# Kernel tuning notes

Measured on AMD Instinct MI355X. Metric: run time of the kernel, lower is better.

## Reference

```python
import jax, jax.numpy as jnp
import numpy as np

N = 50000      # nodes
E = 800000     # edges (avg degree 16)
F_IN = 64      # node_feature_space
H = 64         # hidden_dim
G = 16         # graphs in batch
BN_EPS = 1e-5


def setup_inputs() -> dict:
    key = jax.random.key(0)
    ks = jax.random.split(key, 8)
    x = jax.random.normal(ks[0], (N, F_IN), jnp.float32)
    edge_index = jax.random.randint(ks[1], (2, E), 0, N, dtype=jnp.int64)
    batch = jnp.sort(jax.random.randint(ks[2], (N,), 0, G, dtype=jnp.int64))
    init = lambda k, shp, fan: jax.random.normal(k, shp, jnp.float32) / np.float32(np.sqrt(fan))
    params = dict(
        W1_0=init(ks[3], (F_IN, H), F_IN), b1_0=jnp.zeros((H,), jnp.float32),
        W2_0=init(ks[4], (H, H), H),       b2_0=jnp.zeros((H,), jnp.float32),
        g_0=jnp.ones((H,), jnp.float32),   be_0=jnp.zeros((H,), jnp.float32),
        W1_1=init(ks[5], (H, H), H),       b1_1=jnp.zeros((H,), jnp.float32),
        W2_1=init(ks[6], (H, H), H),       b2_1=jnp.zeros((H,), jnp.float32),
        g_1=jnp.ones((H,), jnp.float32),   be_1=jnp.zeros((H,), jnp.float32),
    )
    return dict(x=x, edge_index=edge_index, batch=batch, **params)


def _gin_layer(x, src, dst, W1, b1, W2, b2, g, be):
    # GINConv (eps=0): h_i = MLP(x_i + sum_{j->i} x_j)
    agg = jax.ops.segment_sum(x[src], dst, num_segments=N)   # [N, d]
    h = x + agg
    h = jnp.maximum(h @ W1 + b1, 0.0) @ W2 + b2              # Linear-ReLU-Linear
    # BatchNorm1d (training-mode batch stats, biased variance as in torch)
    mu = h.mean(axis=0)
    var = h.var(axis=0)
    h = (h - mu) * jax.lax.rsqrt(var + BN_EPS) * g + be
    return jnp.maximum(h, 0.0)                               # ReLU


def reference(x, edge_index, batch,
              W1_0, b1_0, W2_0, b2_0, g_0, be_0,
              W1_1, b1_1, W2_1, b2_1, g_1, be_1):
    src, dst = edge_index[0], edge_index[1]
    x = _gin_layer(x, src, dst, W1_0, b1_0, W2_0, b2_0, g_0, be_0)
    x = _gin_layer(x, src, dst, W1_1, b1_1, W2_1, b2_1, g_1, be_1)
    # global_mean_pool over graph ids
    cnt = jax.ops.segment_sum(jnp.ones((N,), x.dtype), batch, num_segments=G)
    sums = jax.ops.segment_sum(x, batch, num_segments=G)
    h_graph = sums / jnp.maximum(cnt, 1.0)[:, None]
    return (x, h_graph)
```

## Files before the change

### kernel.cpp

```cpp
#include <hip/hip_runtime.h>
#include <hip/hip_bf16.h>


constexpr int NN = 50000;
constexpr int NE = 800000;
constexpr int HD = 64;
constexpr int NG = 16;
constexpr float BN_EPS = 1e-5f;
constexpr int ROWCAP = 64;
constexpr int NPART = 8;
constexpr int PSZ = 6250;

__device__ __forceinline__ int rdl(int v, int l) {
    return __builtin_amdgcn_readlane(v, l);
}

__global__ __launch_bounds__(256)
void prep_kernel(const float* __restrict__ x, __hip_bfloat16* __restrict__ xb,
                 int* __restrict__ cnt, float* __restrict__ stats0,
                 float* __restrict__ stats1, float* __restrict__ psums) {
    int i4 = blockIdx.x * 256 + threadIdx.x;
    if (i4 < NN) cnt[i4] = 0;
    if (blockIdx.x == 0) {
        if (threadIdx.x < 128) stats0[threadIdx.x] = 0.f;
        else stats1[threadIdx.x - 128] = 0.f;
    } else if (blockIdx.x == 1) {
        *(float4*)(psums + threadIdx.x * 4) = make_float4(0.f, 0.f, 0.f, 0.f);
    }
    if (i4 >= NN * HD / 4) return;
    float4 v = *(const float4*)(x + (size_t)i4 * 4);
    union { ushort4 u; __hip_bfloat16 b[4]; } p;
    p.b[0] = __float2bfloat16(v.x);
    p.b[1] = __float2bfloat16(v.y);
    p.b[2] = __float2bfloat16(v.z);
    p.b[3] = __float2bfloat16(v.w);
    *(ushort4*)((unsigned short*)xb + (size_t)i4 * 4) = p.u;
}

__global__ __launch_bounds__(256)
void scatter_kernel(const int* __restrict__ ei, int* __restrict__ cnt,
                    unsigned short* __restrict__ csr) {
    int p = blockIdx.x & 7;
    int chunk = blockIdx.x >> 3;
    int e4 = (chunk * 256 + threadIdx.x) * 4;
    if (e4 >= NE) return;
    int4 s = *(const int4*)(ei + e4);
    int4 d = *(const int4*)(ei + NE + e4);
    int lo = p * PSZ, hi = lo + PSZ;
    int slot;
    if (d.x >= lo && d.x < hi) {
        slot = atomicAdd(&cnt[d.x], 1);
        if (slot < ROWCAP) csr[(d.x << 6) + slot] = (unsigned short)s.x;
    }
    if (d.y >= lo && d.y < hi) {
        slot = atomicAdd(&cnt[d.y], 1);
        if (slot < ROWCAP) csr[(d.y << 6) + slot] = (unsigned short)s.y;
    }
    if (d.z >= lo && d.z < hi) {
        slot = atomicAdd(&cnt[d.z], 1);
        if (slot < ROWCAP) csr[(d.z << 6) + slot] = (unsigned short)s.z;
    }
    if (d.w >= lo && d.w < hi) {
        slot = atomicAdd(&cnt[d.w], 1);
        if (slot < ROWCAP) csr[(d.w << 6) + slot] = (unsigned short)s.w;
    }
}

template <int MODE>
__global__ __launch_bounds__(512)
void layer_kernel(const float* __restrict__ xin, const __hip_bfloat16* __restrict__ xg,
                  const int* __restrict__ cnt, const unsigned short* __restrict__ csr,
                  const float* __restrict__ stats_prev, const float* __restrict__ gp,
                  const float* __restrict__ bep,
                  const float* __restrict__ W1, const float* __restrict__ b1,
                  const float* __restrict__ W2, const float* __restrict__ b2,
                  float* __restrict__ hout, float* __restrict__ stats,
                  __hip_bfloat16* __restrict__ xbr) {
    __shared__ float sh[128 * 65];
    __shared__ float red[2][8][64];
    int tid = threadIdx.x;
    int base = blockIdx.x * 128;
    int w = tid >> 6, lane = tid & 63;
    int wu = __builtin_amdgcn_readfirstlane(w);

    float sc = 1.f, off = 0.f;
    if (MODE == 1) {
        const float inv = 1.f / (float)NN;
        float mu = stats_prev[lane] * inv;
        float var = stats_prev[64 + lane] * inv - mu * mu;
        sc = gp[lane] * rsqrtf(var + BN_EPS);
        off = bep[lane] - mu * sc;
    }

    for (int rl = wu * 16; rl < wu * 16 + 16; rl++) {
        int grow = base + rl;
        float acc = 0.f;
        if (grow < NN) {
            int m = min(cnt[grow], ROWCAP);
            int ids = (int)csr[((size_t)grow << 6) + lane];
            float sv = xin[(size_t)grow * HD + lane];
            acc = (MODE == 1) ? fmaxf(fmaf(sv, sc, off), 0.f) : sv;
            int j = 0;
            float a0 = 0.f, a1 = 0.f, a2 = 0.f, a3 = 0.f;
            float a4 = 0.f, a5 = 0.f, a6 = 0.f, a7 = 0.f;
            for (; j + 8 <= m; j += 8) {
                int n0 = rdl(ids, j);
                int n1 = rdl(ids, j + 1);
                int n2 = rdl(ids, j + 2);
                int n3 = rdl(ids, j + 3);
                int n4 = rdl(ids, j + 4);
                int n5 = rdl(ids, j + 5);
                int n6 = rdl(ids, j + 6);
                int n7 = rdl(ids, j + 7);
                float v0 = __bfloat162float(xg[((size_t)n0 << 6) + lane]);
                float v1 = __bfloat162float(xg[((size_t)n1 << 6) + lane]);
                float v2 = __bfloat162float(xg[((size_t)n2 << 6) + lane]);
                float v3 = __bfloat162float(xg[((size_t)n3 << 6) + lane]);
                float v4 = __bfloat162float(xg[((size_t)n4 << 6) + lane]);
                float v5 = __bfloat162float(xg[((size_t)n5 << 6) + lane]);
                float v6 = __bfloat162float(xg[((size_t)n6 << 6) + lane]);
                float v7 = __bfloat162float(xg[((size_t)n7 << 6) + lane]);
                if (MODE == 1) {
                    a0 += fmaxf(fmaf(v0, sc, off), 0.f);
                    a1 += fmaxf(fmaf(v1, sc, off), 0.f);
                    a2 += fmaxf(fmaf(v2, sc, off), 0.f);
                    a3 += fmaxf(fmaf(v3, sc, off), 0.f);
                    a4 += fmaxf(fmaf(v4, sc, off), 0.f);
                    a5 += fmaxf(fmaf(v5, sc, off), 0.f);
                    a6 += fmaxf(fmaf(v6, sc, off), 0.f);
                    a7 += fmaxf(fmaf(v7, sc, off), 0.f);
                } else {
                    a0 += v0; a1 += v1; a2 += v2; a3 += v3;
                    a4 += v4; a5 += v5; a6 += v6; a7 += v7;
                }
            }
            acc += ((a0 + a1) + (a2 + a3)) + ((a4 + a5) + (a6 + a7));
            for (; j < m; j++) {
                int nb = rdl(ids, j);
                float v = __bfloat162float(xg[((size_t)nb << 6) + lane]);
                acc += (MODE == 1) ? fmaxf(fmaf(v, sc, off), 0.f) : v;
            }
        }
        sh[rl * 65 + lane] = acc;
    }
    __syncthreads();

    float acc0[8], acc1[8];
#pragma unroll
    for (int j = 0; j < 8; j++) { acc0[j] = b1[wu * 8 + j]; acc1[j] = acc0[j]; }
    for (int k = 0; k < 64; k++) {
        float a0 = sh[lane * 65 + k];
        float a1 = sh[(64 + lane) * 65 + k];
        const float4* wr = (const float4*)(W1 + k * 64 + wu * 8);
#pragma unroll
        for (int q = 0; q < 2; q++) {
            float4 wv = wr[q];
            acc0[4 * q + 0] = fmaf(a0, wv.x, acc0[4 * q + 0]);
            acc0[4 * q + 1] = fmaf(a0, wv.y, acc0[4 * q + 1]);
            acc0[4 * q + 2] = fmaf(a0, wv.z, acc0[4 * q + 2]);
            acc0[4 * q + 3] = fmaf(a0, wv.w, acc0[4 * q + 3]);
            acc1[4 * q + 0] = fmaf(a1, wv.x, acc1[4 * q + 0]);
            acc1[4 * q + 1] = fmaf(a1, wv.y, acc1[4 * q + 1]);
            acc1[4 * q + 2] = fmaf(a1, wv.z, acc1[4 * q + 2]);
            acc1[4 * q + 3] = fmaf(a1, wv.w, acc1[4 * q + 3]);
        }
    }
    __syncthreads();

#pragma unroll
    for (int j = 0; j < 8; j++) {
        sh[lane * 65 + wu * 8 + j] = fmaxf(acc0[j], 0.f);
        sh[(64 + lane) * 65 + wu * 8 + j] = fmaxf(acc1[j], 0.f);
    }
    __syncthreads();

#pragma unroll
    for (int j = 0; j < 8; j++) { acc0[j] = b2[wu * 8 + j]; acc1[j] = acc0[j]; }
    for (int k = 0; k < 64; k++) {
        float a0 = sh[lane * 65 + k];
        float a1 = sh[(64 + lane) * 65 + k];
        const float4* wr = (const float4*)(W2 + k * 64 + wu * 8);
#pragma unroll
        for (int q = 0; q < 2; q++) {
            float4 wv = wr[q];
            acc0[4 * q + 0] = fmaf(a0, wv.x, acc0[4 * q + 0]);
            acc0[4 * q + 1] = fmaf(a0, wv.y, acc0[4 * q + 1]);
            acc0[4 * q + 2] = fmaf(a0, wv.z, acc0[4 * q + 2]);
            acc0[4 * q + 3] = fmaf(a0, wv.w, acc0[4 * q + 3]);
            acc1[4 * q + 0] = fmaf(a1, wv.x, acc1[4 * q + 0]);
            acc1[4 * q + 1] = fmaf(a1, wv.y, acc1[4 * q + 1]);
            acc1[4 * q + 2] = fmaf(a1, wv.z, acc1[4 * q + 2]);
            acc1[4 * q + 3] = fmaf(a1, wv.w, acc1[4 * q + 3]);
        }
    }
    __syncthreads();
#pragma unroll
    for (int j = 0; j < 8; j++) {
        sh[lane * 65 + wu * 8 + j] = acc0[j];
        sh[(64 + lane) * 65 + wu * 8 + j] = acc1[j];
    }
    __syncthreads();

#pragma unroll
    for (int i = 0; i < 4; i++) {
        int i4 = tid + 512 * i;
        int row = i4 >> 4, col = (i4 & 15) * 4;
        int grow = base + row;
        if (grow < NN) {
            const float* s = sh + row * 65 + col;
            float4 v = make_float4(s[0], s[1], s[2], s[3]);
            *(float4*)(hout + (size_t)grow * HD + col) = v;
            if (xbr) {
                union { ushort4 u; __hip_bfloat16 b[4]; } p;
                p.b[0] = __float2bfloat16(v.x);
                p.b[1] = __float2bfloat16(v.y);
                p.b[2] = __float2bfloat16(v.z);
                p.b[3] = __float2bfloat16(v.w);
                *(ushort4*)((unsigned short*)xbr + (size_t)grow * HD + col) = p.u;
            }
        }
    }

    {
        float s = 0.f, ss = 0.f;
#pragma unroll
        for (int r = 0; r < 16; r++) {
            int rl = wu * 16 + r;
            float v = (base + rl < NN) ? sh[rl * 65 + lane] : 0.f;
            s += v;
            ss += v * v;
        }
        red[0][wu][lane] = s;
        red[1][wu][lane] = ss;
        __syncthreads();
        if (tid < 64) {
            float S = 0.f;
#pragma unroll
            for (int q = 0; q < 8; q++) S += red[0][q][tid];
            atomicAdd(stats + tid, S);
        } else if (tid < 128) {
            int c = tid - 64;
            float SS = 0.f;
#pragma unroll
            for (int q = 0; q < 8; q++) SS += red[1][q][c];
            atomicAdd(stats + 64 + c, SS);
        }
    }
}

__global__ __launch_bounds__(256)
void norm_kernel(float* h, const float* __restrict__ stats,
                 const float* __restrict__ g, const float* __restrict__ be,
                 const int* __restrict__ batch, float* __restrict__ psums) {
    __shared__ float sg[2][64];
    if (threadIdx.x < 128) sg[threadIdx.x >> 6][threadIdx.x & 63] = 0.f;
    __syncthreads();
    size_t i4 = (size_t)blockIdx.x * 256 + threadIdx.x;
    int row = (int)(i4 >> 4);
    int base_row = blockIdx.x * 16;
    int g0 = batch[base_row];
    size_t off = i4 * 4;
    int col = (int)(off & 63);
    float4 v = *(const float4*)(h + off);
    float4 sm = *(const float4*)(stats + col);
    float4 sq = *(const float4*)(stats + 64 + col);
    float4 gg = *(const float4*)(g + col);
    float4 bb = *(const float4*)(be + col);
    const float inv = 1.f / (float)NN;
    float4 o;
    {
        float mu = sm.x * inv, var = sq.x * inv - mu * mu;
        float sc = gg.x * rsqrtf(var + BN_EPS);
        o.x = fmaxf((v.x - mu) * sc + bb.x, 0.f);
    }
    {
        float mu = sm.y * inv, var = sq.y * inv - mu * mu;
        float sc = gg.y * rsqrtf(var + BN_EPS);
        o.y = fmaxf((v.y - mu) * sc + bb.y, 0.f);
    }
    {
        float mu = sm.z * inv, var = sq.z * inv - mu * mu;
        float sc = gg.z * rsqrtf(var + BN_EPS);
        o.z = fmaxf((v.z - mu) * sc + bb.z, 0.f);
    }
    {
        float mu = sm.w * inv, var = sq.w * inv - mu * mu;
        float sc = gg.w * rsqrtf(var + BN_EPS);
        o.w = fmaxf((v.w - mu) * sc + bb.w, 0.f);
    }
    *(float4*)(h + off) = o;

    int dg = batch[row] - g0;
    if (dg <= 1) {
        atomicAdd(&sg[dg][col + 0], o.x);
        atomicAdd(&sg[dg][col + 1], o.y);
        atomicAdd(&sg[dg][col + 2], o.z);
        atomicAdd(&sg[dg][col + 3], o.w);
    } else {
        int gid = g0 + dg;
        atomicAdd(&psums[gid * HD + col + 0], o.x);
        atomicAdd(&psums[gid * HD + col + 1], o.y);
        atomicAdd(&psums[gid * HD + col + 2], o.z);
        atomicAdd(&psums[gid * HD + col + 3], o.w);
    }
    __syncthreads();
    if (threadIdx.x < 128) {
        int d = threadIdx.x >> 6;
        int c = threadIdx.x & 63;
        float s = sg[d][c];
        if (g0 + d < NG && s != 0.f) atomicAdd(&psums[(g0 + d) * HD + c], s);
    }
}

__device__ __forceinline__ int lower_bound_batch(const int* __restrict__ b, int val) {
    int lo = 0, hi = NN;
    while (lo < hi) {
        int mid = (lo + hi) >> 1;
        if (b[mid] < val) lo = mid + 1;
        else hi = mid;
    }
    return lo;
}

__global__ __launch_bounds__(1024)
void pool_finalize_kernel(const float* __restrict__ sums, const int* __restrict__ batch,
                          float* __restrict__ out) {
    int g = threadIdx.x >> 6;
    int col = threadIdx.x & 63;
    int s = lower_bound_batch(batch, g);
    int e = lower_bound_batch(batch, g + 1);
    float cnt = (float)(e - s);
    out[g * HD + col] = sums[g * HD + col] / fmaxf(cnt, 1.f);
}

extern "C" void kernel_launch(void* const* d_in, const int* in_sizes, int n_in,
                              void* d_out, int out_size, void* d_ws, size_t ws_size,
                              hipStream_t stream) {
    const float* x = (const float*)d_in[0];
    const int* ei = (const int*)d_in[1];
    const int* batch = (const int*)d_in[2];
    const float* W1_0 = (const float*)d_in[3];
    const float* b1_0 = (const float*)d_in[4];
    const float* W2_0 = (const float*)d_in[5];
    const float* b2_0 = (const float*)d_in[6];
    const float* g_0 = (const float*)d_in[7];
    const float* be_0 = (const float*)d_in[8];
    const float* W1_1 = (const float*)d_in[9];
    const float* b1_1 = (const float*)d_in[10];
    const float* W2_1 = (const float*)d_in[11];
    const float* b2_1 = (const float*)d_in[12];
    const float* g_1 = (const float*)d_in[13];
    const float* be_1 = (const float*)d_in[14];

    float* out = (float*)d_out;

    float* stats0 = (float*)d_ws;
    float* stats1 = stats0 + 128;
    float* psums = stats1 + 128;
    int* cnt = (int*)(psums + 1024);
    unsigned short* csr = (unsigned short*)(cnt + NN);
    __hip_bfloat16* xb = (__hip_bfloat16*)(csr + (size_t)NN * ROWCAP);
    __hip_bfloat16* xb2 = xb + (size_t)NN * HD;

    dim3 b256(256);
    dim3 b512(512);
    int layer_grid = (NN + 127) / 128;
    int norm_grid = (NN * HD / 4 + 255) / 256;
    int sct_grid = ((NE + 1023) / 1024) * NPART;

    prep_kernel<<<norm_grid, b256, 0, stream>>>(x, xb, cnt, stats0, stats1, psums);
    scatter_kernel<<<sct_grid, b256, 0, stream>>>(ei, cnt, csr);

    layer_kernel<0><<<layer_grid, b512, 0, stream>>>(
        x, xb, cnt, csr, nullptr, nullptr, nullptr,
        W1_0, b1_0, W2_0, b2_0, out, stats0, xb2);

    layer_kernel<1><<<layer_grid, b512, 0, stream>>>(
        out, xb2, cnt, csr, stats0, g_0, be_0,
        W1_1, b1_1, W2_1, b2_1, out, stats1, (__hip_bfloat16*)nullptr);

    norm_kernel<<<norm_grid, b256, 0, stream>>>(out, stats1, g_1, be_1, batch, psums);
    pool_finalize_kernel<<<1, dim3(1024), 0, stream>>>(psums, batch, out + (size_t)NN * HD);
}
```

Baseline: 278.6 us.

## Shrink layer tile to 64 rows with 1024-thread blocks

Each layer block now covers 64 rows with 16 wavefronts instead of 128 rows with 8 wavefronts. Each wave gathers 4 rows instead of 16, and each thread computes 4 output columns for one row instead of 8 columns for two rows. The aim is more wavefronts in flight to hide the latency of the irregular neighbor gathers, plus a grid twice as large. In exchange, each weight element loaded is reused for only one row, and there are twice as many stats atomics and block-wide barriers across 1024 threads.

```diff
diff --git a/kernel.cpp b/kernel.cpp
--- a/kernel.cpp
+++ b/kernel.cpp
@@ -10,6 +10,7 @@
 constexpr int ROWCAP = 64;
 constexpr int NPART = 8;
 constexpr int PSZ = 6250;
+constexpr int BR = 64;
 
 __device__ __forceinline__ int rdl(int v, int l) {
     return __builtin_amdgcn_readlane(v, l);
@@ -67,7 +68,7 @@
 }
 
 template <int MODE>
-__global__ __launch_bounds__(512)
+__global__ __launch_bounds__(1024)
 void layer_kernel(const float* __restrict__ xin, const __hip_bfloat16* __restrict__ xg,
                   const int* __restrict__ cnt, const unsigned short* __restrict__ csr,
                   const float* __restrict__ stats_prev, const float* __restrict__ gp,
@@ -76,10 +77,10 @@
                   const float* __restrict__ W2, const float* __restrict__ b2,
                   float* __restrict__ hout, float* __restrict__ stats,
                   __hip_bfloat16* __restrict__ xbr) {
-    __shared__ float sh[128 * 65];
-    __shared__ float red[2][8][64];
+    __shared__ float sh[BR * 65];
+    __shared__ float red[2][16][64];
     int tid = threadIdx.x;
-    int base = blockIdx.x * 128;
+    int base = blockIdx.x * BR;
     int w = tid >> 6, lane = tid & 63;
     int wu = __builtin_amdgcn_readfirstlane(w);
 
@@ -92,7 +93,7 @@
         off = bep[lane] - mu * sc;
     }
 
-    for (int rl = wu * 16; rl < wu * 16 + 16; rl++) {
+    for (int rl = wu * 4; rl < wu * 4 + 4; rl++) {
         int grow = base + rl;
         float acc = 0.f;
         if (grow < NN) {
@@ -145,66 +146,42 @@
     }
     __syncthreads();
 
-    float acc0[8], acc1[8];
-#pragma unroll
-    for (int j = 0; j < 8; j++) { acc0[j] = b1[wu * 8 + j]; acc1[j] = acc0[j]; }
+    float acc[4];
+#pragma unroll
+    for (int j = 0; j < 4; j++) acc[j] = b1[wu * 4 + j];
     for (int k = 0; k < 64; k++) {
-        float a0 = sh[lane * 65 + k];
-        float a1 = sh[(64 + lane) * 65 + k];
-        const float4* wr = (const float4*)(W1 + k * 64 + wu * 8);
-#pragma unroll
-        for (int q = 0; q < 2; q++) {
-            float4 wv = wr[q];
-            acc0[4 * q + 0] = fmaf(a0, wv.x, acc0[4 * q + 0]);
-            acc0[4 * q + 1] = fmaf(a0, wv.y, acc0[4 * q + 1]);
-            acc0[4 * q + 2] = fmaf(a0, wv.z, acc0[4 * q + 2]);
-            acc0[4 * q + 3] = fmaf(a0, wv.w, acc0[4 * q + 3]);
-            acc1[4 * q + 0] = fmaf(a1, wv.x, acc1[4 * q + 0]);
-            acc1[4 * q + 1] = fmaf(a1, wv.y, acc1[4 * q + 1]);
-            acc1[4 * q + 2] = fmaf(a1, wv.z, acc1[4 * q + 2]);
-            acc1[4 * q + 3] = fmaf(a1, wv.w, acc1[4 * q + 3]);
-        }
-    }
-    __syncthreads();
-
-#pragma unroll
-    for (int j = 0; j < 8; j++) {
-        sh[lane * 65 + wu * 8 + j] = fmaxf(acc0[j], 0.f);
-        sh[(64 + lane) * 65 + wu * 8 + j] = fmaxf(acc1[j], 0.f);
-    }
-    __syncthreads();
-
-#pragma unroll
-    for (int j = 0; j < 8; j++) { acc0[j] = b2[wu * 8 + j]; acc1[j] = acc0[j]; }
+        float a = sh[lane * 65 + k];
+        float4 wv = *(const float4*)(W1 + k * 64 + wu * 4);
+        acc[0] = fmaf(a, wv.x, acc[0]);
+        acc[1] = fmaf(a, wv.y, acc[1]);
+        acc[2] = fmaf(a, wv.z, acc[2]);
+        acc[3] = fmaf(a, wv.w, acc[3]);
+    }
+    __syncthreads();
+
+#pragma unroll
+    for (int j = 0; j < 4; j++)
+        sh[lane * 65 + wu * 4 + j] = fmaxf(acc[j], 0.f);
+    __syncthreads();
+
+#pragma unroll
+    for (int j = 0; j < 4; j++) acc[j] = b2[wu * 4 + j];
     for (int k = 0; k < 64; k++) {
-        float a0 = sh[lane * 65 + k];
-        float a1 = sh[(64 + lane) * 65 + k];
-        const float4* wr = (const float4*)(W2 + k * 64 + wu * 8);
-#pragma unroll
-        for (int q = 0; q < 2; q++) {
-            float4 wv = wr[q];
-            acc0[4 * q + 0] = fmaf(a0, wv.x, acc0[4 * q + 0]);
-            acc0[4 * q + 1] = fmaf(a0, wv.y, acc0[4 * q + 1]);
-            acc0[4 * q + 2] = fmaf(a0, wv.z, acc0[4 * q + 2]);
-            acc0[4 * q + 3] = fmaf(a0, wv.w, acc0[4 * q + 3]);
-            acc1[4 * q + 0] = fmaf(a1, wv.x, acc1[4 * q + 0]);
-            acc1[4 * q + 1] = fmaf(a1, wv.y, acc1[4 * q + 1]);
-            acc1[4 * q + 2] = fmaf(a1, wv.z, acc1[4 * q + 2]);
-            acc1[4 * q + 3] = fmaf(a1, wv.w, acc1[4 * q + 3]);
-        }
-    }
-    __syncthreads();
-#pragma unroll
-    for (int j = 0; j < 8; j++) {
-        sh[lane * 65 + wu * 8 + j] = acc0[j];
-        sh[(64 + lane) * 65 + wu * 8 + j] = acc1[j];
-    }
-    __syncthreads();
-
-#pragma unroll
-    for (int i = 0; i < 4; i++) {
-        int i4 = tid + 512 * i;
-        int row = i4 >> 4, col = (i4 & 15) * 4;
+        float a = sh[lane * 65 + k];
+        float4 wv = *(const float4*)(W2 + k * 64 + wu * 4);
+        acc[0] = fmaf(a, wv.x, acc[0]);
+        acc[1] = fmaf(a, wv.y, acc[1]);
+        acc[2] = fmaf(a, wv.z, acc[2]);
+        acc[3] = fmaf(a, wv.w, acc[3]);
+    }
+    __syncthreads();
+#pragma unroll
+    for (int j = 0; j < 4; j++)
+        sh[lane * 65 + wu * 4 + j] = acc[j];
+    __syncthreads();
+
+    {
+        int row = tid >> 4, col = (tid & 15) * 4;
         int grow = base + row;
         if (grow < NN) {
             const float* s = sh + row * 65 + col;
@@ -224,8 +201,8 @@
     {
         float s = 0.f, ss = 0.f;
 #pragma unroll
-        for (int r = 0; r < 16; r++) {
-            int rl = wu * 16 + r;
+        for (int r = 0; r < 4; r++) {
+            int rl = wu * 4 + r;
             float v = (base + rl < NN) ? sh[rl * 65 + lane] : 0.f;
             s += v;
             ss += v * v;
@@ -236,13 +213,13 @@
         if (tid < 64) {
             float S = 0.f;
 #pragma unroll
-            for (int q = 0; q < 8; q++) S += red[0][q][tid];
+            for (int q = 0; q < 16; q++) S += red[0][q][tid];
             atomicAdd(stats + tid, S);
         } else if (tid < 128) {
             int c = tid - 64;
             float SS = 0.f;
 #pragma unroll
-            for (int q = 0; q < 8; q++) SS += red[1][q][c];
+            for (int q = 0; q < 16; q++) SS += red[1][q][c];
             atomicAdd(stats + 64 + c, SS);
         }
     }
@@ -363,19 +340,19 @@
     __hip_bfloat16* xb2 = xb + (size_t)NN * HD;
 
     dim3 b256(256);
-    dim3 b512(512);
-    int layer_grid = (NN + 127) / 128;
+    dim3 b1024(1024);
+    int layer_grid = (NN + BR - 1) / BR;
     int norm_grid = (NN * HD / 4 + 255) / 256;
     int sct_grid = ((NE + 1023) / 1024) * NPART;
 
     prep_kernel<<<norm_grid, b256, 0, stream>>>(x, xb, cnt, stats0, stats1, psums);
     scatter_kernel<<<sct_grid, b256, 0, stream>>>(ei, cnt, csr);
 
-    layer_kernel<0><<<layer_grid, b512, 0, stream>>>(
+    layer_kernel<0><<<layer_grid, b1024, 0, stream>>>(
         x, xb, cnt, csr, nullptr, nullptr, nullptr,
         W1_0, b1_0, W2_0, b2_0, out, stats0, xb2);
 
-    layer_kernel<1><<<layer_grid, b512, 0, stream>>>(
+    layer_kernel<1><<<layer_grid, b1024, 0, stream>>>(
         out, xb2, cnt, csr, stats0, g_0, be_0,
         W1_1, b1_1, W2_1, b2_1, out, stats1, (__hip_bfloat16*)nullptr);
 
```

New measurement: 316.0 us. 1.13x slower.
